# Kernel optimization log

Measured on AMD Instinct MI355X. Metric: run time of the kernel, lower is better.

## Reference

```python
import jax, jax.numpy as jnp
import numpy as np

EPS = 1e-5
IOU_SCALE = 10000.0
NEG_TH_ACGT = 3000.0   # int(10000*0.3)
POS_TH_ACGT = 5000.0   # int(10000*0.5)
NUM_POS_RPN = 128
NUM_NEG_RPN = 128

B, N_AC, N_GT = 8, 128 * 128 * 9, 64


def _make_boxes(u):
    # u in [0,1): (yc, xc, sh, sw) -> valid YXYX boxes
    yc, xc = u[..., 0], u[..., 1]
    hh = 0.05 + 0.25 * u[..., 2]
    ww = 0.05 + 0.25 * u[..., 3]
    return jnp.stack([yc - 0.5 * hh, xc - 0.5 * ww, yc + 0.5 * hh, xc + 0.5 * ww], axis=-1)


def setup_inputs() -> dict:
    key = jax.random.key(0)
    k1, k2, k3 = jax.random.split(key, 3)
    anchors = _make_boxes(jax.random.uniform(k1, (N_AC, 4)))
    gt_boxes = _make_boxes(jax.random.uniform(k2, (B, N_GT, 4)))
    deltas = 0.1 * jax.random.normal(k3, (B, N_AC, 4), dtype=jnp.float32)
    return {"anchors": anchors, "gt_boxes": gt_boxes, "deltas": deltas}


def _area(b):
    return jnp.maximum(b[..., 2] - b[..., 0], 0.0) * jnp.maximum(b[..., 3] - b[..., 1], 0.0)


def _iou(ac, gt):
    # ac: (A,4), gt: (B,G,4) -> scaled IoU (B,A,G)
    a = ac[None, :, None, :]
    g = gt[:, None, :, :]
    yi = jnp.maximum(a[..., 0], g[..., 0])
    xi = jnp.maximum(a[..., 1], g[..., 1])
    ya = jnp.minimum(a[..., 2], g[..., 2])
    xa = jnp.minimum(a[..., 3], g[..., 3])
    inter = jnp.maximum(ya - yi, 0.0) * jnp.maximum(xa - xi, 0.0)
    union = _area(a) + _area(g) - inter
    return IOU_SCALE * inter / (union + EPS)


def _bbox2delta(bl, br):
    wr, hr = br[..., 3] - br[..., 1], br[..., 2] - br[..., 0]
    xcr, ycr = br[..., 1] + 0.5 * wr, br[..., 0] + 0.5 * hr
    wr_c, hr_c = jnp.maximum(wr, EPS), jnp.maximum(hr, EPS)
    wl, hl = bl[..., 3] - bl[..., 1], bl[..., 2] - bl[..., 0]
    xcl, ycl = bl[..., 1] + 0.5 * wl, bl[..., 0] + 0.5 * hl
    d = jnp.stack([(xcl - xcr) / wr_c, (ycl - ycr) / hr_c,
                   jnp.log(wl / wr_c), jnp.log(hl / hr_c)], axis=-1)
    return jnp.clip(d, -10.0, 10.0)


def _delta2bbox(base, diff):
    wb, hb = base[..., 3] - base[..., 1], base[..., 2] - base[..., 0]
    xc = base[..., 1] + 0.5 * wb + wb * diff[..., 0]
    yc = base[..., 0] + 0.5 * hb + hb * diff[..., 1]
    w_ = wb * jnp.exp(diff[..., 2])
    h_ = hb * jnp.exp(diff[..., 3])
    # from_xywh -> YXYX
    return jnp.stack([yc - 0.5 * h_, xc - 0.5 * w_, yc + 0.5 * h_, xc + 0.5 * w_], axis=-1)


def _sample_mask(mask, num, key):
    th = num / (jnp.sum(mask, axis=-1, keepdims=True) + 1e-6)
    rand = jax.random.uniform(key, mask.shape, dtype=jnp.float32)
    return jnp.where(rand < th, 1.0, 0.0) * mask


def reference(anchors, gt_boxes, deltas):
    ious = _iou(anchors, gt_boxes)                 # (B, A, G)
    best_iou = jnp.max(ious, axis=-1)              # (B, A)
    best_idx = jnp.argmax(ious, axis=-1)           # (B, A)
    gt_best = jnp.take_along_axis(
        gt_boxes, jnp.broadcast_to(best_idx[:, :, None], best_idx.shape + (4,)), axis=1)

    pos = best_iou > POS_TH_ACGT
    neg = best_iou < NEG_TH_ACGT
    # fg: matched GT box; bkg: all -2; ignore: all -1
    bx_tgt = jnp.where(pos[..., None], gt_best,
                       jnp.where(neg[..., None], -2.0, -1.0))

    coor_sum = jnp.sum(bx_tgt, axis=-1)
    kp, kn = jax.random.split(jax.random.key(42))
    mask_pos = _sample_mask(jnp.where(coor_sum > -4.0, 1.0, 0.0), NUM_POS_RPN, kp)
    mask_neg = _sample_mask(jnp.where(coor_sum <= -8.0, 1.0, 0.0), NUM_NEG_RPN, kn)

    ac_b = jnp.broadcast_to(anchors[None], bx_tgt.shape)
    # safe left operand so log() stays finite for non-positive anchors
    bx_tgt_safe = jnp.where(pos[..., None], bx_tgt, ac_b)
    del_tgt = _bbox2delta(bx_tgt_safe, ac_b) * mask_pos[..., None]   # (B, A, 4)

    proposals = _delta2bbox(anchors[None], deltas)                    # (B, A, 4)
    return jnp.concatenate([proposals, del_tgt], axis=-1)            # (B, A, 8)
```

## Files before the change

### kernel.cpp

```cpp
#include <hip/hip_runtime.h>
#include <stdint.h>

#define NAC 147456
#define NGT 64
#define NB  8
#define APT 3
#define BLK 256
#define GX  (NAC / (BLK * APT))

__host__ __device__ static inline uint32_t tf_rotl(uint32_t x, uint32_t d) {
  return (x << d) | (x >> (32u - d));
}

__host__ __device__ static inline void threefry2x32(
    uint32_t k0, uint32_t k1, uint32_t x0, uint32_t x1,
    uint32_t* o0, uint32_t* o1)
{
  const uint32_t ks2 = k0 ^ k1 ^ 0x1BD11BDAu;
  x0 += k0; x1 += k1;
#define TFR(r) { x0 += x1; x1 = tf_rotl(x1, (r)); x1 ^= x0; }
  TFR(13u) TFR(15u) TFR(26u) TFR(6u)   x0 += k1;  x1 += ks2 + 1u;
  TFR(17u) TFR(29u) TFR(16u) TFR(24u)  x0 += ks2; x1 += k0 + 2u;
  TFR(13u) TFR(15u) TFR(26u) TFR(6u)   x0 += k0;  x1 += k1 + 3u;
  TFR(17u) TFR(29u) TFR(16u) TFR(24u)  x0 += k1;  x1 += ks2 + 4u;
  TFR(13u) TFR(15u) TFR(26u) TFR(6u)   x0 += ks2; x1 += k0 + 5u;
#undef TFR
  *o0 = x0; *o1 = x1;
}

__device__ static inline void bbox2delta_store(
    const float4& a, const float4& g, float* dst)
{
  const float wr  = a.w - a.y,          hr  = a.z - a.x;
  const float xcr = a.y + 0.5f * wr,    ycr = a.x + 0.5f * hr;
  const float wrc = fmaxf(wr, 1e-5f),   hrc = fmaxf(hr, 1e-5f);
  const float wl  = g.w - g.y,          hl  = g.z - g.x;
  const float xcl = g.y + 0.5f * wl,    ycl = g.x + 0.5f * hl;
  float4 r;
  r.x = fminf(fmaxf((xcl - xcr) / wrc, -10.0f), 10.0f);
  r.y = fminf(fmaxf((ycl - ycr) / hrc, -10.0f), 10.0f);
  r.z = fminf(fmaxf(__logf(wl / wrc),  -10.0f), 10.0f);
  r.w = fminf(fmaxf(__logf(hl / hrc),  -10.0f), 10.0f);
  *reinterpret_cast<float4*>(dst) = r;
}

template <bool USE_FLAGS>
__global__ __launch_bounds__(BLK) void k1_classify(
    const float* __restrict__ anchors,
    const float* __restrict__ gt,
    const float* __restrict__ deltas,
    float* __restrict__ out,
    int* __restrict__ cnt_blk,
    unsigned char* __restrict__ flags)
{
  __shared__ __align__(16) float4 gbox[NGT];
  __shared__ __align__(16) float  garea[NGT];
  __shared__ __align__(16) float  gae[NGT];
  __shared__ int s_cnt;
  const int b   = blockIdx.y;
  const int tid = threadIdx.x;

  if (tid == 0) s_cnt = 0;
  if (tid < NGT) {
    float4 g = reinterpret_cast<const float4*>(gt)[b * NGT + tid];
    const float ga = fmaxf(g.z - g.x, 0.0f) * fmaxf(g.w - g.y, 0.0f);
    gbox[tid]  = g;
    garea[tid] = ga;
    gae[tid]   = ga + 1e-5f;
  }
  __syncthreads();

  const int base = blockIdx.x * (BLK * APT) + tid;

  float4 a[APT];
  float  areaA[APT], num[APT], Tb[APT];
  int    bidx[APT];
#pragma unroll
  for (int t = 0; t < APT; ++t) {
    a[t] = reinterpret_cast<const float4*>(anchors)[base + t * BLK];
    areaA[t] = fmaxf(a[t].z - a[t].x, 0.0f) * fmaxf(a[t].w - a[t].y, 0.0f);
    num[t]  = 0.0f;
    Tb[t]   = 1.0f;
    bidx[t] = 0;
  }

  for (int jj = 0; jj < NGT; jj += 4) {
    const float4 te4 = *reinterpret_cast<const float4*>(&gae[jj]);
    const float4 g0 = gbox[jj + 0];
    const float4 g1 = gbox[jj + 1];
    const float4 g2 = gbox[jj + 2];
    const float4 g3 = gbox[jj + 3];
    const float4 gs[4] = { g0, g1, g2, g3 };
#pragma unroll
    for (int u = 0; u < 4; ++u) {
      const float4 g  = gs[u];
      const float  te = (&te4.x)[u];
      const int    j  = jj + u;
#pragma unroll
      for (int t = 0; t < APT; ++t) {
        float yi = fmaxf(a[t].x, g.x);
        float xi = fmaxf(a[t].y, g.y);
        float ya = fminf(a[t].z, g.z);
        float xa = fminf(a[t].w, g.w);
        float inter = fmaxf(ya - yi, 0.0f) * fmaxf(xa - xi, 0.0f);
        float Tj = areaA[t] + te;
        bool upd = inter * Tb[t] > num[t] * Tj;
        num[t]  = upd ? inter : num[t];
        Tb[t]   = upd ? Tj    : Tb[t];
        bidx[t] = upd ? j     : bidx[t];
      }
    }
  }

  int npos = 0;
#pragma unroll
  for (int t = 0; t < APT; ++t) {
    const int i = base + t * BLK;
    const float gaB = garea[bidx[t]];
    const float den = ((areaA[t] + gaB) - num[t]) + 1e-5f;
    const float best_iou = (10000.0f * num[t]) / den;
    const bool pos = best_iou > 5000.0f;

    const float4 d = reinterpret_cast<const float4*>(deltas)[b * NAC + i];
    const float wb = a[t].w - a[t].y, hb = a[t].z - a[t].x;
    const float xc = a[t].y + 0.5f * wb + wb * d.x;
    const float yc = a[t].x + 0.5f * hb + hb * d.y;
    const float w_ = wb * __expf(d.z);
    const float h_ = hb * __expf(d.w);

    float* rowp = out + ((size_t)b * NAC + i) * 8;
    reinterpret_cast<float4*>(rowp)[0] =
        make_float4(yc - 0.5f * h_, xc - 0.5f * w_, yc + 0.5f * h_, xc + 0.5f * w_);
    if (USE_FLAGS) {
      reinterpret_cast<float4*>(rowp)[1] = make_float4(0.f, 0.f, 0.f, 0.f);
      flags[(size_t)b * NAC + i] = pos ? (unsigned char)(bidx[t] + 1) : 0u;
    } else {
      reinterpret_cast<float4*>(rowp)[1] =
          make_float4(pos ? (float)(bidx[t] + 1) : 0.0f, 0.f, 0.f, 0.f);
    }

    unsigned long long m = __ballot(pos);
    if ((tid & 63) == 0) npos += (int)__popcll(m);
  }
  if ((tid & 63) == 0 && npos)
    atomicAdd(&s_cnt, npos);
  __syncthreads();

  if (tid == 0) {
    if (USE_FLAGS) cnt_blk[b * GX + blockIdx.x] = s_cnt;
    else if (s_cnt) atomicAdd(&cnt_blk[b], s_cnt);
  }
}

__global__ __launch_bounds__(256) void k2_flags(
    const float* __restrict__ anchors,
    const float* __restrict__ gt,
    float* __restrict__ out,
    const int* __restrict__ cnt_blk,
    const unsigned char* __restrict__ flags,
    uint32_t kp0, uint32_t kp1)
{
  __shared__ int s_tot;
  const int b   = blockIdx.y;
  const int tid = threadIdx.x;

  if (tid == 0) s_tot = 0;
  __syncthreads();
  if (tid < GX) atomicAdd(&s_tot, cnt_blk[b * GX + tid]);
  __syncthreads();
  const float th = 128.0f / ((float)s_tot + 1e-6f);

  const int chunk = blockIdx.x * 256 + tid;
  uint4 fv = reinterpret_cast<const uint4*>(flags + (size_t)b * NAC)[chunk];
  if ((fv.x | fv.y | fv.z | fv.w) == 0u) return;

  const uint32_t words[4] = { fv.x, fv.y, fv.z, fv.w };
  const int base_i = chunk * 16;

#pragma unroll
  for (int w = 0; w < 4; ++w) {
    uint32_t wd = words[w];
    while (wd) {
      const int byte = __ffs(wd) / 8;
      const int fl   = (wd >> (byte * 8)) & 0xFF;
      wd &= ~(0xFFu << (byte * 8));
      const int i = base_i + w * 4 + byte;
      const int f = b * NAC + i;

      uint32_t o0, o1;
      threefry2x32(kp0, kp1, 0u, (uint32_t)f, &o0, &o1);
      const uint32_t bits = o0 ^ o1;
      union { uint32_t u; float flt; } cv;
      cv.u = (bits >> 9) | 0x3F800000u;
      if (cv.flt - 1.0f < th) {
        const float4 a = reinterpret_cast<const float4*>(anchors)[i];
        const float4 g = reinterpret_cast<const float4*>(gt)[b * NGT + (fl - 1)];
        bbox2delta_store(a, g, out + (size_t)f * 8 + 4);
      }
    }
  }
}

__global__ __launch_bounds__(256) void k2_fallback(
    const float* __restrict__ anchors,
    const float* __restrict__ gt,
    float* __restrict__ out,
    const int* __restrict__ counts,
    uint32_t kp0, uint32_t kp1)
{
  const int b = blockIdx.y;
  const int i = blockIdx.x * 256 + threadIdx.x;
  const int f = b * NAC + i;
  float* rowp = out + (size_t)f * 8;

  const float flag = rowp[4];
  if (flag == 0.0f) return;

  const float th = 128.0f / ((float)counts[b] + 1e-6f);

  uint32_t o0, o1;
  threefry2x32(kp0, kp1, 0u, (uint32_t)f, &o0, &o1);
  const uint32_t bits = o0 ^ o1;
  union { uint32_t u; float flt; } cv;
  cv.u = (bits >> 9) | 0x3F800000u;

  if (cv.flt - 1.0f < th) {
    const float4 a = reinterpret_cast<const float4*>(anchors)[i];
    const float4 g = reinterpret_cast<const float4*>(gt)[b * NGT + ((int)flag - 1)];
    bbox2delta_store(a, g, rowp + 4);
  } else {
    reinterpret_cast<float4*>(rowp)[1] = make_float4(0.f, 0.f, 0.f, 0.f);
  }
}

extern "C" void kernel_launch(void* const* d_in, const int* in_sizes, int n_in,
                              void* d_out, int out_size, void* d_ws, size_t ws_size,
                              hipStream_t stream)
{
  const float* anchors = (const float*)d_in[0];
  const float* gt      = (const float*)d_in[1];
  const float* deltas  = (const float*)d_in[2];
  float* out  = (float*)d_out;
  int* cnt_blk = (int*)d_ws;
  unsigned char* flags = (unsigned char*)d_ws + 8192;

  const bool use_flags = ws_size >= (size_t)(8192 + NB * NAC);

  uint32_t kp0, kp1;
  threefry2x32(0u, 42u, 0u, 0u, &kp0, &kp1);

  dim3 g1(GX, NB);
  if (use_flags) {
    k1_classify<true><<<g1, dim3(BLK), 0, stream>>>(anchors, gt, deltas, out,
                                                    cnt_blk, flags);
    dim3 g2(NAC / 16 / 256, NB);
    k2_flags<<<g2, dim3(256), 0, stream>>>(anchors, gt, out, cnt_blk, flags,
                                           kp0, kp1);
  } else {
    hipMemsetAsync(cnt_blk, 0, NB * sizeof(int), stream);
    k1_classify<false><<<g1, dim3(BLK), 0, stream>>>(anchors, gt, deltas, out,
                                                     cnt_blk, nullptr);
    dim3 g2(NAC / 256, NB);
    k2_fallback<<<g2, dim3(256), 0, stream>>>(anchors, gt, out, cnt_blk,
                                              kp0, kp1);
  }
}
```

Baseline: 116.2 us.

## Fuse classify and sampling into one cooperative kernel with grid sync

```diff
diff --git a/kernel.cpp b/kernel.cpp
--- a/kernel.cpp
+++ b/kernel.cpp
@@ -1,5 +1,8 @@
 #include <hip/hip_runtime.h>
+#include <hip/hip_cooperative_groups.h>
 #include <stdint.h>
+
+namespace cg = cooperative_groups;
 
 #define NAC 147456
 #define NGT 64
@@ -28,8 +31,7 @@
   *o0 = x0; *o1 = x1;
 }
 
-__device__ static inline void bbox2delta_store(
-    const float4& a, const float4& g, float* dst)
+__device__ static inline float4 bbox2delta_calc(const float4& a, const float4& g)
 {
   const float wr  = a.w - a.y,          hr  = a.z - a.x;
   const float xcr = a.y + 0.5f * wr,    ycr = a.x + 0.5f * hr;
@@ -41,17 +43,16 @@
   r.y = fminf(fmaxf((ycl - ycr) / hrc, -10.0f), 10.0f);
   r.z = fminf(fmaxf(__logf(wl / wrc),  -10.0f), 10.0f);
   r.w = fminf(fmaxf(__logf(hl / hrc),  -10.0f), 10.0f);
-  *reinterpret_cast<float4*>(dst) = r;
-}
-
-template <bool USE_FLAGS>
-__global__ __launch_bounds__(BLK) void k1_classify(
+  return r;
+}
+
+__global__ __launch_bounds__(BLK) void k_fused(
     const float* __restrict__ anchors,
     const float* __restrict__ gt,
     const float* __restrict__ deltas,
     float* __restrict__ out,
-    int* __restrict__ cnt_blk,
-    unsigned char* __restrict__ flags)
+    int* __restrict__ counts,
+    uint32_t kp0, uint32_t kp1)
 {
   __shared__ __align__(16) float4 gbox[NGT];
   __shared__ __align__(16) float  garea[NGT];
@@ -112,6 +113,7 @@
     }
   }
 
+  int posm = 0;
   int npos = 0;
 #pragma unroll
   for (int t = 0; t < APT; ++t) {
@@ -120,6 +122,7 @@
     const float den = ((areaA[t] + gaB) - num[t]) + 1e-5f;
     const float best_iou = (10000.0f * num[t]) / den;
     const bool pos = best_iou > 5000.0f;
+    posm |= (pos ? 1 : 0) << t;
 
     const float4 d = reinterpret_cast<const float4*>(deltas)[b * NAC + i];
     const float wb = a[t].w - a[t].y, hb = a[t].z - a[t].x;
@@ -131,13 +134,6 @@
     float* rowp = out + ((size_t)b * NAC + i) * 8;
     reinterpret_cast<float4*>(rowp)[0] =
         make_float4(yc - 0.5f * h_, xc - 0.5f * w_, yc + 0.5f * h_, xc + 0.5f * w_);
-    if (USE_FLAGS) {
-      reinterpret_cast<float4*>(rowp)[1] = make_float4(0.f, 0.f, 0.f, 0.f);
-      flags[(size_t)b * NAC + i] = pos ? (unsigned char)(bidx[t] + 1) : 0u;
-    } else {
-      reinterpret_cast<float4*>(rowp)[1] =
-          make_float4(pos ? (float)(bidx[t] + 1) : 0.0f, 0.f, 0.f, 0.f);
-    }
 
     unsigned long long m = __ballot(pos);
     if ((tid & 63) == 0) npos += (int)__popcll(m);
@@ -145,60 +141,131 @@
   if ((tid & 63) == 0 && npos)
     atomicAdd(&s_cnt, npos);
   __syncthreads();
-
-  if (tid == 0) {
-    if (USE_FLAGS) cnt_blk[b * GX + blockIdx.x] = s_cnt;
-    else if (s_cnt) atomicAdd(&cnt_blk[b], s_cnt);
-  }
-}
-
-__global__ __launch_bounds__(256) void k2_flags(
-    const float* __restrict__ anchors,
-    const float* __restrict__ gt,
-    float* __restrict__ out,
-    const int* __restrict__ cnt_blk,
-    const unsigned char* __restrict__ flags,
-    uint32_t kp0, uint32_t kp1)
-{
-  __shared__ int s_tot;
-  const int b   = blockIdx.y;
-  const int tid = threadIdx.x;
-
-  if (tid == 0) s_tot = 0;
-  __syncthreads();
-  if (tid < GX) atomicAdd(&s_tot, cnt_blk[b * GX + tid]);
-  __syncthreads();
-  const float th = 128.0f / ((float)s_tot + 1e-6f);
-
-  const int chunk = blockIdx.x * 256 + tid;
-  uint4 fv = reinterpret_cast<const uint4*>(flags + (size_t)b * NAC)[chunk];
-  if ((fv.x | fv.y | fv.z | fv.w) == 0u) return;
-
-  const uint32_t words[4] = { fv.x, fv.y, fv.z, fv.w };
-  const int base_i = chunk * 16;
-
-#pragma unroll
-  for (int w = 0; w < 4; ++w) {
-    uint32_t wd = words[w];
-    while (wd) {
-      const int byte = __ffs(wd) / 8;
-      const int fl   = (wd >> (byte * 8)) & 0xFF;
-      wd &= ~(0xFFu << (byte * 8));
-      const int i = base_i + w * 4 + byte;
-      const int f = b * NAC + i;
-
+  if (tid == 0 && s_cnt)
+    atomicAdd(&counts[b], s_cnt);
+
+  cg::this_grid().sync();
+
+  const int tot = __hip_atomic_load(&counts[b], __ATOMIC_RELAXED,
+                                    __HIP_MEMORY_SCOPE_AGENT);
+  const float th = 128.0f / ((float)tot + 1e-6f);
+
+#pragma unroll
+  for (int t = 0; t < APT; ++t) {
+    const int i = base + t * BLK;
+    const int f = b * NAC + i;
+    float4 r = make_float4(0.f, 0.f, 0.f, 0.f);
+    if ((posm >> t) & 1) {
       uint32_t o0, o1;
       threefry2x32(kp0, kp1, 0u, (uint32_t)f, &o0, &o1);
       const uint32_t bits = o0 ^ o1;
       union { uint32_t u; float flt; } cv;
       cv.u = (bits >> 9) | 0x3F800000u;
       if (cv.flt - 1.0f < th) {
-        const float4 a = reinterpret_cast<const float4*>(anchors)[i];
-        const float4 g = reinterpret_cast<const float4*>(gt)[b * NGT + (fl - 1)];
-        bbox2delta_store(a, g, out + (size_t)f * 8 + 4);
+        const float4 g = gbox[bidx[t]];
+        r = bbox2delta_calc(a[t], g);
       }
     }
-  }
+    reinterpret_cast<float4*>(out + (size_t)f * 8)[1] = r;
+  }
+}
+
+__global__ __launch_bounds__(BLK) void k1_classify(
+    const float* __restrict__ anchors,
+    const float* __restrict__ gt,
+    const float* __restrict__ deltas,
+    float* __restrict__ out,
+    int* __restrict__ counts)
+{
+  __shared__ __align__(16) float4 gbox[NGT];
+  __shared__ __align__(16) float  garea[NGT];
+  __shared__ __align__(16) float  gae[NGT];
+  __shared__ int s_cnt;
+  const int b   = blockIdx.y;
+  const int tid = threadIdx.x;
+
+  if (tid == 0) s_cnt = 0;
+  if (tid < NGT) {
+    float4 g = reinterpret_cast<const float4*>(gt)[b * NGT + tid];
+    const float ga = fmaxf(g.z - g.x, 0.0f) * fmaxf(g.w - g.y, 0.0f);
+    gbox[tid]  = g;
+    garea[tid] = ga;
+    gae[tid]   = ga + 1e-5f;
+  }
+  __syncthreads();
+
+  const int base = blockIdx.x * (BLK * APT) + tid;
+
+  float4 a[APT];
+  float  areaA[APT], num[APT], Tb[APT];
+  int    bidx[APT];
+#pragma unroll
+  for (int t = 0; t < APT; ++t) {
+    a[t] = reinterpret_cast<const float4*>(anchors)[base + t * BLK];
+    areaA[t] = fmaxf(a[t].z - a[t].x, 0.0f) * fmaxf(a[t].w - a[t].y, 0.0f);
+    num[t]  = 0.0f;
+    Tb[t]   = 1.0f;
+    bidx[t] = 0;
+  }
+
+  for (int jj = 0; jj < NGT; jj += 4) {
+    const float4 te4 = *reinterpret_cast<const float4*>(&gae[jj]);
+    const float4 g0 = gbox[jj + 0];
+    const float4 g1 = gbox[jj + 1];
+    const float4 g2 = gbox[jj + 2];
+    const float4 g3 = gbox[jj + 3];
+    const float4 gs[4] = { g0, g1, g2, g3 };
+#pragma unroll
+    for (int u = 0; u < 4; ++u) {
+      const float4 g  = gs[u];
+      const float  te = (&te4.x)[u];
+      const int    j  = jj + u;
+#pragma unroll
+      for (int t = 0; t < APT; ++t) {
+        float yi = fmaxf(a[t].x, g.x);
+        float xi = fmaxf(a[t].y, g.y);
+        float ya = fminf(a[t].z, g.z);
+        float xa = fminf(a[t].w, g.w);
+        float inter = fmaxf(ya - yi, 0.0f) * fmaxf(xa - xi, 0.0f);
+        float Tj = areaA[t] + te;
+        bool upd = inter * Tb[t] > num[t] * Tj;
+        num[t]  = upd ? inter : num[t];
+        Tb[t]   = upd ? Tj    : Tb[t];
+        bidx[t] = upd ? j     : bidx[t];
+      }
+    }
+  }
+
+  int npos = 0;
+#pragma unroll
+  for (int t = 0; t < APT; ++t) {
+    const int i = base + t * BLK;
+    const float gaB = garea[bidx[t]];
+    const float den = ((areaA[t] + gaB) - num[t]) + 1e-5f;
+    const float best_iou = (10000.0f * num[t]) / den;
+    const bool pos = best_iou > 5000.0f;
+
+    const float4 d = reinterpret_cast<const float4*>(deltas)[b * NAC + i];
+    const float wb = a[t].w - a[t].y, hb = a[t].z - a[t].x;
+    const float xc = a[t].y + 0.5f * wb + wb * d.x;
+    const float yc = a[t].x + 0.5f * hb + hb * d.y;
+    const float w_ = wb * __expf(d.z);
+    const float h_ = hb * __expf(d.w);
+
+    float* rowp = out + ((size_t)b * NAC + i) * 8;
+    reinterpret_cast<float4*>(rowp)[0] =
+        make_float4(yc - 0.5f * h_, xc - 0.5f * w_, yc + 0.5f * h_, xc + 0.5f * w_);
+    reinterpret_cast<float4*>(rowp)[1] =
+        make_float4(pos ? (float)(bidx[t] + 1) : 0.0f, 0.f, 0.f, 0.f);
+
+    unsigned long long m = __ballot(pos);
+    if ((tid & 63) == 0) npos += (int)__popcll(m);
+  }
+  if ((tid & 63) == 0 && npos)
+    atomicAdd(&s_cnt, npos);
+  __syncthreads();
+
+  if (tid == 0 && s_cnt) atomicAdd(&counts[b], s_cnt);
 }
 
 __global__ __launch_bounds__(256) void k2_fallback(
@@ -227,7 +294,8 @@
   if (cv.flt - 1.0f < th) {
     const float4 a = reinterpret_cast<const float4*>(anchors)[i];
     const float4 g = reinterpret_cast<const float4*>(gt)[b * NGT + ((int)flag - 1)];
-    bbox2delta_store(a, g, rowp + 4);
+    float4 r = bbox2delta_calc(a, g);
+    *reinterpret_cast<float4*>(rowp + 4) = r;
   } else {
     reinterpret_cast<float4*>(rowp)[1] = make_float4(0.f, 0.f, 0.f, 0.f);
   }
@@ -240,28 +308,37 @@
   const float* anchors = (const float*)d_in[0];
   const float* gt      = (const float*)d_in[1];
   const float* deltas  = (const float*)d_in[2];
-  float* out  = (float*)d_out;
-  int* cnt_blk = (int*)d_ws;
-  unsigned char* flags = (unsigned char*)d_ws + 8192;
-
-  const bool use_flags = ws_size >= (size_t)(8192 + NB * NAC);
+  float* out   = (float*)d_out;
+  int* counts  = (int*)d_ws;
 
   uint32_t kp0, kp1;
   threefry2x32(0u, 42u, 0u, 0u, &kp0, &kp1);
 
-  dim3 g1(GX, NB);
-  if (use_flags) {
-    k1_classify<true><<<g1, dim3(BLK), 0, stream>>>(anchors, gt, deltas, out,
-                                                    cnt_blk, flags);
-    dim3 g2(NAC / 16 / 256, NB);
-    k2_flags<<<g2, dim3(256), 0, stream>>>(anchors, gt, out, cnt_blk, flags,
-                                           kp0, kp1);
-  } else {
-    hipMemsetAsync(cnt_blk, 0, NB * sizeof(int), stream);
-    k1_classify<false><<<g1, dim3(BLK), 0, stream>>>(anchors, gt, deltas, out,
-                                                     cnt_blk, nullptr);
+  static int coop_ok = -1;
+  if (coop_ok < 0) {
+    int dev = 0, c = 0;
+    hipGetDevice(&dev);
+    hipDeviceGetAttribute(&c, hipDeviceAttributeCooperativeLaunch, dev);
+    coop_ok = c;
+  }
+
+  hipMemsetAsync(counts, 0, NB * sizeof(int), stream);
+
+  bool launched = false;
+  if (coop_ok) {
+    void* params[] = { (void*)&anchors, (void*)&gt, (void*)&deltas,
+                       (void*)&out, (void*)&counts, (void*)&kp0, (void*)&kp1 };
+    hipError_t e = hipLaunchCooperativeKernel(
+        reinterpret_cast<void*>(k_fused), dim3(GX, NB), dim3(BLK),
+        params, 0, stream);
+    launched = (e == hipSuccess);
+    if (!launched) coop_ok = 0;
+  }
+  if (!launched) {
+    dim3 g1(GX, NB);
+    k1_classify<<<g1, dim3(BLK), 0, stream>>>(anchors, gt, deltas, out, counts);
     dim3 g2(NAC / 256, NB);
-    k2_fallback<<<g2, dim3(256), 0, stream>>>(anchors, gt, out, cnt_blk,
+    k2_fallback<<<g2, dim3(256), 0, stream>>>(anchors, gt, out, counts,
                                               kp0, kp1);
   }
 }
```

Measured after the change: 119.6 us. 2.9% more time.

## Replace per-anchor flag array with compacted positive-anchor list

Applied to the files above, without the earlier changes.

```diff
diff --git a/kernel.cpp b/kernel.cpp
--- a/kernel.cpp
+++ b/kernel.cpp
@@ -7,6 +7,7 @@
 #define APT 3
 #define BLK 256
 #define GX  (NAC / (BLK * APT))
+#define LCAP 36864
 
 __host__ __device__ static inline uint32_t tf_rotl(uint32_t x, uint32_t d) {
   return (x << d) | (x >> (32u - d));
@@ -44,19 +45,20 @@
   *reinterpret_cast<float4*>(dst) = r;
 }
 
-template <bool USE_FLAGS>
+template <bool USE_LIST>
 __global__ __launch_bounds__(BLK) void k1_classify(
     const float* __restrict__ anchors,
     const float* __restrict__ gt,
     const float* __restrict__ deltas,
     float* __restrict__ out,
-    int* __restrict__ cnt_blk,
-    unsigned char* __restrict__ flags)
+    int* __restrict__ cnt,
+    uint32_t* __restrict__ list)
 {
   __shared__ __align__(16) float4 gbox[NGT];
   __shared__ __align__(16) float  garea[NGT];
   __shared__ __align__(16) float  gae[NGT];
   __shared__ int s_cnt;
+  __shared__ int s_base;
   const int b   = blockIdx.y;
   const int tid = threadIdx.x;
 
@@ -102,7 +104,7 @@
         float xi = fmaxf(a[t].y, g.y);
         float ya = fminf(a[t].z, g.z);
         float xa = fminf(a[t].w, g.w);
-        float inter = fmaxf(ya - yi, 0.0f) * fmaxf(xa - xi, 0.0f);
+        float inter = fmaxf(ya - yi, 0.0f) * (xa - xi);
         float Tj = areaA[t] + te;
         bool upd = inter * Tb[t] > num[t] * Tj;
         num[t]  = upd ? inter : num[t];
@@ -112,7 +114,7 @@
     }
   }
 
-  int npos = 0;
+  int slot[APT];
 #pragma unroll
   for (int t = 0; t < APT; ++t) {
     const int i = base + t * BLK;
@@ -120,6 +122,7 @@
     const float den = ((areaA[t] + gaB) - num[t]) + 1e-5f;
     const float best_iou = (10000.0f * num[t]) / den;
     const bool pos = best_iou > 5000.0f;
+    slot[t] = pos ? atomicAdd(&s_cnt, 1) : -1;
 
     const float4 d = reinterpret_cast<const float4*>(deltas)[b * NAC + i];
     const float wb = a[t].w - a[t].y, hb = a[t].z - a[t].x;
@@ -131,72 +134,63 @@
     float* rowp = out + ((size_t)b * NAC + i) * 8;
     reinterpret_cast<float4*>(rowp)[0] =
         make_float4(yc - 0.5f * h_, xc - 0.5f * w_, yc + 0.5f * h_, xc + 0.5f * w_);
-    if (USE_FLAGS) {
+    if (USE_LIST) {
       reinterpret_cast<float4*>(rowp)[1] = make_float4(0.f, 0.f, 0.f, 0.f);
-      flags[(size_t)b * NAC + i] = pos ? (unsigned char)(bidx[t] + 1) : 0u;
     } else {
       reinterpret_cast<float4*>(rowp)[1] =
           make_float4(pos ? (float)(bidx[t] + 1) : 0.0f, 0.f, 0.f, 0.f);
     }
-
-    unsigned long long m = __ballot(pos);
-    if ((tid & 63) == 0) npos += (int)__popcll(m);
-  }
-  if ((tid & 63) == 0 && npos)
-    atomicAdd(&s_cnt, npos);
+  }
   __syncthreads();
-
   if (tid == 0) {
-    if (USE_FLAGS) cnt_blk[b * GX + blockIdx.x] = s_cnt;
-    else if (s_cnt) atomicAdd(&cnt_blk[b], s_cnt);
-  }
-}
-
-__global__ __launch_bounds__(256) void k2_flags(
+    s_base = s_cnt ? atomicAdd(&cnt[b], s_cnt) : 0;
+  }
+  __syncthreads();
+
+  if (USE_LIST) {
+#pragma unroll
+    for (int t = 0; t < APT; ++t) {
+      if (slot[t] >= 0) {
+        const int e = s_base + slot[t];
+        if (e < LCAP) {
+          const int i = base + t * BLK;
+          list[b * LCAP + e] = (uint32_t)i | ((uint32_t)bidx[t] << 18);
+        }
+      }
+    }
+  }
+}
+
+__global__ __launch_bounds__(256) void k2_list(
     const float* __restrict__ anchors,
     const float* __restrict__ gt,
     float* __restrict__ out,
-    const int* __restrict__ cnt_blk,
-    const unsigned char* __restrict__ flags,
+    const int* __restrict__ cnt,
+    const uint32_t* __restrict__ list,
     uint32_t kp0, uint32_t kp1)
 {
-  __shared__ int s_tot;
   const int b   = blockIdx.y;
   const int tid = threadIdx.x;
 
-  if (tid == 0) s_tot = 0;
-  __syncthreads();
-  if (tid < GX) atomicAdd(&s_tot, cnt_blk[b * GX + tid]);
-  __syncthreads();
-  const float th = 128.0f / ((float)s_tot + 1e-6f);
-
-  const int chunk = blockIdx.x * 256 + tid;
-  uint4 fv = reinterpret_cast<const uint4*>(flags + (size_t)b * NAC)[chunk];
-  if ((fv.x | fv.y | fv.z | fv.w) == 0u) return;
-
-  const uint32_t words[4] = { fv.x, fv.y, fv.z, fv.w };
-  const int base_i = chunk * 16;
-
-#pragma unroll
-  for (int w = 0; w < 4; ++w) {
-    uint32_t wd = words[w];
-    while (wd) {
-      const int byte = __ffs(wd) / 8;
-      const int fl   = (wd >> (byte * 8)) & 0xFF;
-      wd &= ~(0xFFu << (byte * 8));
-      const int i = base_i + w * 4 + byte;
-      const int f = b * NAC + i;
-
-      uint32_t o0, o1;
-      threefry2x32(kp0, kp1, 0u, (uint32_t)f, &o0, &o1);
-      const uint32_t bits = o0 ^ o1;
-      union { uint32_t u; float flt; } cv;
-      cv.u = (bits >> 9) | 0x3F800000u;
-      if (cv.flt - 1.0f < th) {
-        const float4 a = reinterpret_cast<const float4*>(anchors)[i];
-        const float4 g = reinterpret_cast<const float4*>(gt)[b * NGT + (fl - 1)];
-        bbox2delta_store(a, g, out + (size_t)f * 8 + 4);
-      }
+  int tot = cnt[b];
+  const float th = 128.0f / ((float)tot + 1e-6f);
+  if (tot > LCAP) tot = LCAP;
+
+  for (int e = blockIdx.x * 256 + tid; e < tot; e += 16 * 256) {
+    const uint32_t p = list[b * LCAP + e];
+    const int i  = (int)(p & 0x3FFFFu);
+    const int fl = (int)(p >> 18);
+    const int f  = b * NAC + i;
+
+    uint32_t o0, o1;
+    threefry2x32(kp0, kp1, 0u, (uint32_t)f, &o0, &o1);
+    const uint32_t bits = o0 ^ o1;
+    union { uint32_t u; float flt; } cv;
+    cv.u = (bits >> 9) | 0x3F800000u;
+    if (cv.flt - 1.0f < th) {
+      const float4 a = reinterpret_cast<const float4*>(anchors)[i];
+      const float4 g = reinterpret_cast<const float4*>(gt)[b * NGT + fl];
+      bbox2delta_store(a, g, out + (size_t)f * 8 + 4);
     }
   }
 }
@@ -241,27 +235,28 @@
   const float* gt      = (const float*)d_in[1];
   const float* deltas  = (const float*)d_in[2];
   float* out  = (float*)d_out;
-  int* cnt_blk = (int*)d_ws;
-  unsigned char* flags = (unsigned char*)d_ws + 8192;
-
-  const bool use_flags = ws_size >= (size_t)(8192 + NB * NAC);
+  int* cnt = (int*)d_ws;
+  uint32_t* list = (uint32_t*)((char*)d_ws + 256);
+
+  const bool use_list = ws_size >= (size_t)(256 + NB * LCAP * 4);
 
   uint32_t kp0, kp1;
   threefry2x32(0u, 42u, 0u, 0u, &kp0, &kp1);
 
+  hipMemsetAsync(cnt, 0, NB * sizeof(int), stream);
+
   dim3 g1(GX, NB);
-  if (use_flags) {
+  if (use_list) {
     k1_classify<true><<<g1, dim3(BLK), 0, stream>>>(anchors, gt, deltas, out,
-                                                    cnt_blk, flags);
-    dim3 g2(NAC / 16 / 256, NB);
-    k2_flags<<<g2, dim3(256), 0, stream>>>(anchors, gt, out, cnt_blk, flags,
-                                           kp0, kp1);
+                                                    cnt, list);
+    dim3 g2(16, NB);
+    k2_list<<<g2, dim3(256), 0, stream>>>(anchors, gt, out, cnt, list,
+                                          kp0, kp1);
   } else {
-    hipMemsetAsync(cnt_blk, 0, NB * sizeof(int), stream);
     k1_classify<false><<<g1, dim3(BLK), 0, stream>>>(anchors, gt, deltas, out,
-                                                     cnt_blk, nullptr);
+                                                     cnt, nullptr);
     dim3 g2(NAC / 256, NB);
-    k2_fallback<<<g2, dim3(256), 0, stream>>>(anchors, gt, out, cnt_blk,
+    k2_fallback<<<g2, dim3(256), 0, stream>>>(anchors, gt, out, cnt,
                                               kp0, kp1);
   }
 }
```

Result: no change. 115.1 us (-1.0%).
